# Performance work log

Hardware: AMD Instinct MI355X
Metric: run time of the kernel (lower is better)

Reference implementation:

```python
import jax, jax.numpy as jnp
import numpy as np

TAU = 0.5

def setup_inputs() -> dict:
    key = jax.random.key(0)
    kx, ky = jax.random.split(key)
    B, H = 8192, 256
    x = jax.random.normal(kx, (B, H), dtype=jnp.float32)
    y = jax.random.normal(ky, (B, H), dtype=jnp.float32)
    return {"x": x, "y": y}

def reference(x, y):
    # L2-normalize rows
    x_norm = x / jnp.linalg.norm(x, axis=1, keepdims=True)
    y_norm = y / jnp.linalg.norm(y, axis=1, keepdims=True)
    xy_norm = jnp.concatenate([x_norm, y_norm], axis=0)  # [2N, H]
    yx_norm = jnp.concatenate([y_norm, x_norm], axis=0)  # [2N, H]
    # [2N, 2N] cosine-similarity matrix (dominant memory traffic)
    sim_mat_1 = xy_norm @ xy_norm.T
    exp_mat = jnp.exp(sim_mat_1 / TAU)
    exp_row_sum = jnp.sum(exp_mat, axis=1)
    exp_diag = jnp.diagonal(exp_mat)
    denominator = exp_row_sum - exp_diag
    # diag(xy_norm @ yx_norm.T) is the row-wise dot product (avoids redundant NxN matmul)
    pos_sim = jnp.sum(xy_norm * yx_norm, axis=1)
    numerator = jnp.exp(pos_sim / TAU)
    nt_xent = -jnp.log(numerator / denominator)
    return jnp.mean(nt_xent)
```

## Files before the change

kernel.cpp:

```cpp
#include <hip/hip_runtime.h>
#include <hip/hip_bf16.h>
#include <math.h>

constexpr int NROWS = 8192;
constexpr int HDIM  = 256;
constexpr int N2    = 16384;
constexpr int BM    = 128;
constexpr int BK    = 32;
constexpr int NCHUNK = HDIM / BK;
constexpr int NTILE = N2 / BM;
constexpr int NBLK  = NTILE * (NTILE + 1) / 2;

constexpr float PRESCALE = 1.69864357f;

typedef __attribute__((ext_vector_type(4))) float floatx4;
typedef __attribute__((ext_vector_type(8))) short shortx8;

__device__ __forceinline__ void async_copy16(const void* gptr, void* lptr) {
    __builtin_amdgcn_global_load_lds(
        (const __attribute__((address_space(1))) unsigned int*)gptr,
        (__attribute__((address_space(3))) unsigned int*)lptr, 16, 0, 0);
}

#define WAIT_VM4()   __builtin_amdgcn_s_waitcnt(0x0F74)
#define WAIT_VM0()   __builtin_amdgcn_s_waitcnt(0x0F70)
#define WAIT_LGKM0() __builtin_amdgcn_s_waitcnt(0xC07F)
#define MEMFENCE()   __asm__ __volatile__("" ::: "memory")
#define RAW_BARRIER() do { MEMFENCE(); __builtin_amdgcn_s_barrier(); MEMFENCE(); } while (0)

__global__ __launch_bounds__(256) void normalize_kernel(
    const float* __restrict__ x, const float* __restrict__ y,
    __hip_bfloat16* __restrict__ Z, float* __restrict__ pos,
    float* __restrict__ rowsum, float* __restrict__ out)
{
    const int wave = threadIdx.x >> 6, lane = threadIdx.x & 63;
    const int row  = blockIdx.x * 4 + wave;

    const float4 xv = ((const float4*)x)[row * 64 + lane];
    const float4 yv = ((const float4*)y)[row * 64 + lane];

    float sx  = xv.x*xv.x + xv.y*xv.y + xv.z*xv.z + xv.w*xv.w;
    float sy  = yv.x*yv.x + yv.y*yv.y + yv.z*yv.z + yv.w*yv.w;
    float sxy = xv.x*yv.x + xv.y*yv.y + xv.z*yv.z + xv.w*yv.w;
    #pragma unroll
    for (int m = 1; m < 64; m <<= 1) {
        sx  += __shfl_xor(sx,  m);
        sy  += __shfl_xor(sy,  m);
        sxy += __shfl_xor(sxy, m);
    }
    const float rxn = rsqrtf(sx), ryn = rsqrtf(sy);
    const float rx = rxn * PRESCALE, ry = ryn * PRESCALE;

    union { ushort4 u; __hip_bfloat16 h[4]; } zx, zy;
    zx.h[0] = __float2bfloat16(xv.x * rx); zx.h[1] = __float2bfloat16(xv.y * rx);
    zx.h[2] = __float2bfloat16(xv.z * rx); zx.h[3] = __float2bfloat16(xv.w * rx);
    zy.h[0] = __float2bfloat16(yv.x * ry); zy.h[1] = __float2bfloat16(yv.y * ry);
    zy.h[2] = __float2bfloat16(yv.z * ry); zy.h[3] = __float2bfloat16(yv.w * ry);
    ((ushort4*)Z)[row * 64 + lane]             = zx.u;
    ((ushort4*)Z)[(row + NROWS) * 64 + lane]   = zy.u;

    if (lane == 0) {
        const float p = sxy * rxn * ryn;
        pos[row]         = p;
        pos[row + NROWS] = p;
    }
    const int gt = blockIdx.x * 256 + threadIdx.x;
    if (gt < N2) rowsum[gt] = 0.f;
    if (gt == 0) out[0] = 0.f;
}

__global__ __launch_bounds__(256, 4) void simgemm_kernel(
    const __hip_bfloat16* __restrict__ Z, float* __restrict__ rowsum)
{
    const int b = blockIdx.x;
    int bi = (int)((257.0f - sqrtf(66049.0f - 8.0f * (float)b)) * 0.5f);
    int cum = bi * (257 - bi) / 2;
    if (b < cum)      { bi--; cum = bi * (257 - bi) / 2; }
    else { const int cn = (bi + 1) * (256 - bi) / 2;
           if (b >= cn) { bi++; cum = cn; } }
    const int bj = bi + (b - cum);
    const bool diag = (bi == bj);

    __shared__ alignas(16) __hip_bfloat16 tiles[4 * BM * BK];
    __shared__ float rs[BM];
    __shared__ float cs[BM];
    __hip_bfloat16* tA = tiles;
    __hip_bfloat16* tB = tiles + 2 * BM * BK;

    const int tid  = threadIdx.x;
    const int wave = tid >> 6;
    const int lane = tid & 63;
    const int wm   = wave & 1;
    const int wn   = wave >> 1;
    const int g    = lane >> 4;
    const int m15  = lane & 15;

    if (tid < BM) { rs[tid] = 0.f; cs[tid] = 0.f; }

    const int st_r0  = wave * 32 + (lane >> 2);
    const int st_c   = (lane & 3) ^ ((lane >> 3) & 3);
    const __hip_bfloat16* gA0 = Z + (size_t)(bi * BM + st_r0) * HDIM + st_c * 8;
    const __hip_bfloat16* gA1 = gA0 + 16 * HDIM;
    const __hip_bfloat16* gB0 = Z + (size_t)(bj * BM + st_r0) * HDIM + st_c * 8;
    const __hip_bfloat16* gB1 = gB0 + 16 * HDIM;
    __hip_bfloat16* lA0 = tA + (wave * 32) * BK;
    __hip_bfloat16* lA1 = tA + (wave * 32 + 16) * BK;
    __hip_bfloat16* lB0 = tB + (wave * 32) * BK;
    __hip_bfloat16* lB1 = tB + (wave * 32 + 16) * BK;

    const int sw = g ^ ((m15 >> 1) & 3);
    const __hip_bfloat16* rA = tA + (wm * 64 + m15) * BK + sw * 8;
    const __hip_bfloat16* rB = tB + (wn * 64 + m15) * BK + sw * 8;

    floatx4 acc[4][4] = {};

    #define STAGE(ck, buf)  do {                                            \
        async_copy16(gA0 + (ck) * BK, lA0 + (buf) * BM * BK);               \
        async_copy16(gA1 + (ck) * BK, lA1 + (buf) * BM * BK);               \
        async_copy16(gB0 + (ck) * BK, lB0 + (buf) * BM * BK);               \
        async_copy16(gB1 + (ck) * BK, lB1 + (buf) * BM * BK);               \
    } while (0)

    STAGE(0, 0);

    #pragma unroll
    for (int ck = 0; ck < NCHUNK; ++ck) {
        const int cur = ck & 1;
        if (ck + 1 < NCHUNK) { STAGE(ck + 1, cur ^ 1); WAIT_VM4(); }
        else                 { WAIT_VM0(); }
        RAW_BARRIER();

        shortx8 af[4], bfr[4];
        #pragma unroll
        for (int f = 0; f < 4; ++f) {
            af[f]  = *(const shortx8*)(rA + cur * BM * BK + f * 16 * BK);
            bfr[f] = *(const shortx8*)(rB + cur * BM * BK + f * 16 * BK);
        }
        #pragma unroll
        for (int fm = 0; fm < 4; ++fm)
            #pragma unroll
            for (int fn = 0; fn < 4; ++fn)
                acc[fm][fn] = __builtin_amdgcn_mfma_f32_16x16x32_bf16(
                    af[fm], bfr[fn], acc[fm][fn], 0, 0, 0);

        WAIT_LGKM0();
        RAW_BARRIER();
    }
    #undef STAGE

    float rp[4][4] = {{0.f}};
    float cp[4]    = {0.f};

    if (!diag) {
        #pragma unroll
        for (int fm = 0; fm < 4; ++fm)
            #pragma unroll
            for (int fn = 0; fn < 4; ++fn) {
                const floatx4 a = acc[fm][fn];
                #pragma unroll
                for (int q = 0; q < 4; ++q) {
                    const float e = __builtin_amdgcn_exp2f(a[q]);
                    rp[fm][q] += e;
                    cp[fn]    += e;
                }
            }
    } else {
        #pragma unroll
        for (int fm = 0; fm < 4; ++fm)
            #pragma unroll
            for (int fn = 0; fn < 4; ++fn) {
                const floatx4 a = acc[fm][fn];
                const int cl = wn * 64 + fn * 16 + m15;
                #pragma unroll
                for (int q = 0; q < 4; ++q) {
                    const int rl = wm * 64 + fm * 16 + g * 4 + q;
                    float e = __builtin_amdgcn_exp2f(a[q]);
                    if (cl <= rl) e = 0.f;
                    rp[fm][q] += e;
                    cp[fn]    += e;
                }
            }
    }

    #pragma unroll
    for (int mask = 1; mask < 16; mask <<= 1)
        #pragma unroll
        for (int fm = 0; fm < 4; ++fm)
            #pragma unroll
            for (int q = 0; q < 4; ++q)
                rp[fm][q] += __shfl_xor(rp[fm][q], mask);
    if (m15 == 0) {
        #pragma unroll
        for (int fm = 0; fm < 4; ++fm)
            #pragma unroll
            for (int q = 0; q < 4; ++q)
                atomicAdd(&rs[wm * 64 + fm * 16 + g * 4 + q], rp[fm][q]);
    }

    #pragma unroll
    for (int mask = 16; mask < 64; mask <<= 1)
        #pragma unroll
        for (int fn = 0; fn < 4; ++fn)
            cp[fn] += __shfl_xor(cp[fn], mask);
    if (g == 0) {
        #pragma unroll
        for (int fn = 0; fn < 4; ++fn)
            atomicAdd(&cs[wn * 64 + fn * 16 + m15], cp[fn]);
    }

    __syncthreads();
    if (tid < BM) {
        atomicAdd(&rowsum[(size_t)bi * BM + tid], rs[tid]);
        atomicAdd(&rowsum[(size_t)bj * BM + tid], cs[tid]);
    }
}

__global__ __launch_bounds__(1024) void finalize_kernel(
    const float* __restrict__ rowsum, const float* __restrict__ pos,
    float* __restrict__ out)
{
    const int i = threadIdx.x + blockIdx.x * 1024;
    float s = logf(rowsum[i]) - 2.0f * pos[i];
    #pragma unroll
    for (int off = 32; off; off >>= 1) s += __shfl_down(s, off);
    __shared__ float sh[16];
    const int lt = threadIdx.x;
    if ((lt & 63) == 0) sh[lt >> 6] = s;
    __syncthreads();
    if (lt == 0) {
        float tot = 0.f;
        #pragma unroll
        for (int w = 0; w < 16; ++w) tot += sh[w];
        atomicAdd(out, tot / (float)N2);
    }
}

extern "C" void kernel_launch(void* const* d_in, const int* in_sizes, int n_in,
                              void* d_out, int out_size, void* d_ws, size_t ws_size,
                              hipStream_t stream)
{
    const float* x = (const float*)d_in[0];
    const float* y = (const float*)d_in[1];

    __hip_bfloat16* Z = (__hip_bfloat16*)d_ws;
    float* rowsum = (float*)((char*)d_ws + (size_t)N2 * HDIM * sizeof(__hip_bfloat16));
    float* pos    = rowsum + N2;

    normalize_kernel<<<NROWS / 4, 256, 0, stream>>>(x, y, Z, pos, rowsum, (float*)d_out);
    simgemm_kernel<<<NBLK, 256, 0, stream>>>(Z, rowsum);
    finalize_kernel<<<N2 / 1024, 1024, 0, stream>>>(rowsum, pos, (float*)d_out);
}
```

Measured before the change: 179.9 us.

## Triple-buffer LDS staging and remap triangular tile order for L2 locality

Switches the K-loop from double to triple buffering, keeping two async global-to-LDS chunk loads in flight while computing on a third. This aims to hide global load latency better. It also replaces the linear upper-triangle block enumeration with a grouped mapping: blocks sharing the low three bits work on a 16x16 tile super-block, so concurrently scheduled blocks reuse the same rows in cache. The cost is more LDS per block and launch bounds lowered from 4 to 3 blocks per CU, which reduces occupancy.

Result: faster. 176.3 us (-2.0%).

```diff
diff --git a/kernel.cpp b/kernel.cpp
--- a/kernel.cpp
+++ b/kernel.cpp
@@ -22,6 +22,7 @@
         (__attribute__((address_space(3))) unsigned int*)lptr, 16, 0, 0);
 }
 
+#define WAIT_VM8()   __builtin_amdgcn_s_waitcnt(0x0F78)
 #define WAIT_VM4()   __builtin_amdgcn_s_waitcnt(0x0F74)
 #define WAIT_VM0()   __builtin_amdgcn_s_waitcnt(0x0F70)
 #define WAIT_LGKM0() __builtin_amdgcn_s_waitcnt(0xC07F)
@@ -69,23 +70,42 @@
     if (gt == 0) out[0] = 0.f;
 }
 
-__global__ __launch_bounds__(256, 4) void simgemm_kernel(
+__global__ __launch_bounds__(256, 3) void simgemm_kernel(
     const __hip_bfloat16* __restrict__ Z, float* __restrict__ rowsum)
 {
     const int b = blockIdx.x;
-    int bi = (int)((257.0f - sqrtf(66049.0f - 8.0f * (float)b)) * 0.5f);
-    int cum = bi * (257 - bi) / 2;
-    if (b < cum)      { bi--; cum = bi * (257 - bi) / 2; }
-    else { const int cn = (bi + 1) * (256 - bi) / 2;
-           if (b >= cn) { bi++; cum = cn; } }
-    const int bj = bi + (b - cum);
+    const int k = b & 7;
+    const int m = b >> 3;
+    int bi, bj;
+    if (m < 136) {
+        int ti = (int)((33.0f - sqrtf(1089.0f - 8.0f * (float)m)) * 0.5f);
+        if (m < ti * (33 - ti) / 2) ti--;
+        else if (m >= (ti + 1) * (32 - ti) / 2) ti++;
+        const int tj = ti + (m - ti * (33 - ti) / 2);
+        bi = k * 16 + ti;
+        bj = k * 16 + tj;
+    } else {
+        const int m2 = m - 136;
+        const int hh = m2 >> 7;
+        const int r  = m2 & 127;
+        const int h  = hh * 8 + k;
+        const int q  = h >> 1;
+        const int sub = h & 1;
+        int gi = 0;
+        #pragma unroll
+        for (int t = 6; t > 0; --t)
+            if (q >= t * (15 - t) / 2) { gi = t; break; }
+        const int gj = gi + 1 + (q - gi * (15 - gi) / 2);
+        bi = gi * 16 + sub * 8 + (r >> 4);
+        bj = gj * 16 + (r & 15);
+    }
     const bool diag = (bi == bj);
 
-    __shared__ alignas(16) __hip_bfloat16 tiles[4 * BM * BK];
+    __shared__ alignas(16) __hip_bfloat16 tiles[6 * BM * BK];
     __shared__ float rs[BM];
     __shared__ float cs[BM];
     __hip_bfloat16* tA = tiles;
-    __hip_bfloat16* tB = tiles + 2 * BM * BK;
+    __hip_bfloat16* tB = tiles + BM * BK;
 
     const int tid  = threadIdx.x;
     const int wave = tid >> 6;
@@ -114,27 +134,30 @@
 
     floatx4 acc[4][4] = {};
 
-    #define STAGE(ck, buf)  do {                                            \
-        async_copy16(gA0 + (ck) * BK, lA0 + (buf) * BM * BK);               \
-        async_copy16(gA1 + (ck) * BK, lA1 + (buf) * BM * BK);               \
-        async_copy16(gB0 + (ck) * BK, lB0 + (buf) * BM * BK);               \
-        async_copy16(gB1 + (ck) * BK, lB1 + (buf) * BM * BK);               \
+    #define STAGE(ck)  do {                                                  \
+        const int _o = ((ck) % 3) * 2 * BM * BK;                             \
+        async_copy16(gA0 + (ck) * BK, lA0 + _o);                             \
+        async_copy16(gA1 + (ck) * BK, lA1 + _o);                             \
+        async_copy16(gB0 + (ck) * BK, lB0 + _o);                             \
+        async_copy16(gB1 + (ck) * BK, lB1 + _o);                             \
     } while (0)
 
-    STAGE(0, 0);
-
-    #pragma unroll
-    for (int ck = 0; ck < NCHUNK; ++ck) {
-        const int cur = ck & 1;
-        if (ck + 1 < NCHUNK) { STAGE(ck + 1, cur ^ 1); WAIT_VM4(); }
-        else                 { WAIT_VM0(); }
+    STAGE(0);
+    STAGE(1);
+
+    #pragma unroll
+    for (int s = 0; s < NCHUNK; ++s) {
+        if (s + 2 < NCHUNK)      { STAGE(s + 2); WAIT_VM8(); }
+        else if (s + 1 < NCHUNK) { WAIT_VM4(); }
+        else                     { WAIT_VM0(); }
         RAW_BARRIER();
 
+        const int bo = (s % 3) * 2 * BM * BK;
         shortx8 af[4], bfr[4];
         #pragma unroll
         for (int f = 0; f < 4; ++f) {
-            af[f]  = *(const shortx8*)(rA + cur * BM * BK + f * 16 * BK);
-            bfr[f] = *(const shortx8*)(rB + cur * BM * BK + f * 16 * BK);
+            af[f]  = *(const shortx8*)(rA + bo + f * 16 * BK);
+            bfr[f] = *(const shortx8*)(rB + bo + f * 16 * BK);
         }
         #pragma unroll
         for (int fm = 0; fm < 4; ++fm)
```
